# Kernel optimization log

Measured on AMD Instinct MI355X. Metric: run time of the kernel, lower is better.

## Reference

```python
import jax, jax.numpy as jnp
import numpy as np

B, S, H, NH = 2, 2048, 1024, 16
HD = H // NH
ROTARY_DIM = 64
EPS = 1e-5
MINUS_INF = -10000.0


def _apply_rotary(q, k, rotary_dim):
    # q, k: [B, S, NH, HD]; GPT-NeoX style rotate_half on first rotary_dim dims
    pos = jnp.arange(S, dtype=jnp.float32)
    inv_freq = 1.0 / (10000.0 ** (jnp.arange(0, rotary_dim, 2, dtype=jnp.float32) / rotary_dim))
    freqs = pos[:, None] * inv_freq[None, :]                      # [S, rd/2]
    cos = jnp.concatenate([jnp.cos(freqs)] * 2, -1)[None, :, None, :]  # [1,S,1,rd]
    sin = jnp.concatenate([jnp.sin(freqs)] * 2, -1)[None, :, None, :]

    def rot(t):
        t_rot, t_pass = t[..., :rotary_dim], t[..., rotary_dim:]
        t1, t2 = jnp.split(t_rot, 2, axis=-1)
        rotated = jnp.concatenate([-t2, t1], axis=-1)
        return jnp.concatenate([t_rot * cos + rotated * sin, t_pass], axis=-1)

    return rot(q), rot(k)


def setup_inputs() -> dict:
    key = jax.random.key(0)
    ks = jax.random.split(key, 6)
    w_scale = 0.02
    return {
        "x": jax.random.normal(ks[0], (B, S, H), jnp.float32),
        "input_mask": jnp.ones((B, S), jnp.int32),
        "norm_w": jnp.ones((H,), jnp.float32),
        "norm_b": jnp.zeros((H,), jnp.float32),
        "attn_qkvw": jax.random.normal(ks[1], (H, 3 * H), jnp.float32) * w_scale,
        "attn_qkvb": jax.random.normal(ks[2], (3 * H,), jnp.float32) * w_scale,
        "attn_ow": jax.random.normal(ks[3], (H, H), jnp.float32) * w_scale,
        "attn_ob": jax.random.normal(ks[4], (H,), jnp.float32) * w_scale,
    }


def reference(x, input_mask, norm_w, norm_b, attn_qkvw, attn_qkvb, attn_ow, attn_ob):
    # pre-layernorm (qkv_gemm path with config.pre_layer_norm)
    mu = x.mean(-1, keepdims=True)
    var = x.var(-1, keepdims=True)
    xn = (x - mu) * jax.lax.rsqrt(var + EPS) * norm_w + norm_b

    # fused QKV projection
    qkv = xn @ attn_qkvw + attn_qkvb                       # [B,S,3H]
    q, k, v = jnp.split(qkv, 3, axis=-1)
    q = q.reshape(B, S, NH, HD)
    k = k.reshape(B, S, NH, HD)
    v = v.reshape(B, S, NH, HD)

    # rotary embedding on q,k
    q, k = _apply_rotary(q, k, ROTARY_DIM)

    # scaled scores + mask bias (1 - mask) * -10000 + triangular masking
    scale = 1.0 / np.sqrt(HD).astype(np.float32)
    scores = jnp.einsum("bqhd,bkhd->bhqk", q, k) * scale   # [B,NH,S,S]
    mask_bias = (1.0 - input_mask.astype(scores.dtype)) * MINUS_INF
    scores = scores + mask_bias[:, None, None, :]
    causal = jnp.tril(jnp.ones((S, S), bool))
    scores = jnp.where(causal[None, None], scores, MINUS_INF)

    probs = jax.nn.softmax(scores, axis=-1)
    ctx = jnp.einsum("bhqk,bkhd->bqhd", probs, v).reshape(B, S, H)

    # output projection (vector_matmul + bias)
    return ctx @ attn_ow + attn_ob
```

## Files before the change

kernel.cpp:

```cpp
#include <hip/hip_runtime.h>
#include <hip/hip_bf16.h>

#define B_  2
#define S_  2048
#define H_  1024
#define NH_ 16
#define HD_ 64
#define T_  (B_*S_)
#define H3_ (3*H_)

typedef float  floatx4 __attribute__((ext_vector_type(4)));
typedef __bf16 bf16x8  __attribute__((ext_vector_type(8)));

__device__ inline unsigned short f2bf_rn(float f) {
    union { float f; unsigned int u; } v; v.f = f;
    unsigned int u = v.u;
    u += 0x7fffu + ((u >> 16) & 1u);
    return (unsigned short)(u >> 16);
}
__device__ inline floatx4 fzero4() { floatx4 v; v[0]=0.f; v[1]=0.f; v[2]=0.f; v[3]=0.f; return v; }

__device__ inline float bf2f(unsigned short u) {
    union { unsigned int i; float f; } x; x.i = ((unsigned int)u) << 16; return x.f;
}

__device__ inline unsigned int cvtpk_bf16(float lo, float hi) {
    unsigned int r;
    asm("v_cvt_pk_bf16_f32 %0, %1, %2" : "=v"(r) : "v"(lo), "v"(hi));
    return r;
}
__device__ inline float bfsum2(unsigned int u) {
    union { unsigned int i; float f; } a, c;
    a.i = u << 16; c.i = u & 0xffff0000u;
    return a.f + c.f;
}

__device__ inline void gload_lds16(const unsigned short* g, unsigned short* l) {
    __builtin_amdgcn_global_load_lds((const __attribute__((address_space(1))) unsigned int*)g,
                                     (__attribute__((address_space(3))) unsigned int*)l,
                                     16, 0, 0);
}

#define TLD 72
__global__ __launch_bounds__(256) void cvt_both_k(const float* __restrict__ qkvw,
                                                  const float* __restrict__ ow,
                                                  unsigned short* __restrict__ qkvwT,
                                                  unsigned short* __restrict__ owT) {
    __shared__ unsigned short Ts[64 * TLD];
    int id = blockIdx.x;
    const float* W; unsigned short* Wt; int N, nb, kb;
    if (id < 768) { W = qkvw; Wt = qkvwT; N = H3_; nb = (id % 48) * 64; kb = (id / 48) * 64; }
    else { id -= 768; W = ow; Wt = owT; N = H_; nb = (id % 16) * 64; kb = (id / 16) * 64; }
    const int K = H_;
    const int tid = threadIdx.x;
    #pragma unroll
    for (int p = 0; p < 4; p++) {
        const int krow = kb + p * 16 + (tid >> 4);
        const int ncol = (tid & 15) * 4;
        const float4 w = *reinterpret_cast<const float4*>(&W[(size_t)krow * N + nb + ncol]);
        Ts[(ncol + 0) * TLD + p * 16 + (tid >> 4)] = f2bf_rn(w.x);
        Ts[(ncol + 1) * TLD + p * 16 + (tid >> 4)] = f2bf_rn(w.y);
        Ts[(ncol + 2) * TLD + p * 16 + (tid >> 4)] = f2bf_rn(w.z);
        Ts[(ncol + 3) * TLD + p * 16 + (tid >> 4)] = f2bf_rn(w.w);
    }
    __syncthreads();
    #pragma unroll
    for (int p = 0; p < 2; p++) {
        const int n = (tid >> 3) + p * 32;
        const int k8 = (tid & 7) * 8;
        const uint4 v = *reinterpret_cast<const uint4*>(&Ts[n * TLD + k8]);
        *reinterpret_cast<uint4*>(&Wt[(size_t)(nb + n) * K + kb + k8]) = v;
    }
}

__global__ __launch_bounds__(256) void layernorm_k(const float* __restrict__ x,
                                                   const float* __restrict__ w,
                                                   const float* __restrict__ b,
                                                   unsigned short* __restrict__ xn) {
    const int t   = blockIdx.x;
    const int tid = threadIdx.x;
    const float4 v = reinterpret_cast<const float4*>(x + (size_t)t * H_)[tid];
    float s  = v.x + v.y + v.z + v.w;
    float s2 = v.x*v.x + v.y*v.y + v.z*v.z + v.w*v.w;
    for (int off = 32; off > 0; off >>= 1) {
        s  += __shfl_down(s,  off, 64);
        s2 += __shfl_down(s2, off, 64);
    }
    __shared__ float red[8];
    const int wave = tid >> 6, lane = tid & 63;
    if (lane == 0) { red[wave] = s; red[4 + wave] = s2; }
    __syncthreads();
    if (tid == 0) {
        red[0] = red[0] + red[1] + red[2] + red[3];
        red[4] = red[4] + red[5] + red[6] + red[7];
    }
    __syncthreads();
    const float mean = red[0] * (1.f / H_);
    const float var  = red[4] * (1.f / H_) - mean * mean;
    const float rstd = rsqrtf(var + 1e-5f);
    const float4 wv = reinterpret_cast<const float4*>(w)[tid];
    const float4 bv = reinterpret_cast<const float4*>(b)[tid];
    ushort4 o = make_ushort4(f2bf_rn((v.x - mean) * rstd * wv.x + bv.x),
                             f2bf_rn((v.y - mean) * rstd * wv.y + bv.y),
                             f2bf_rn((v.z - mean) * rstd * wv.z + bv.z),
                             f2bf_rn((v.w - mean) * rstd * wv.w + bv.w));
    reinterpret_cast<ushort4*>(xn + (size_t)t * H_)[tid] = o;
}

#define BM 128
#define BN 128

__device__ inline void gemm_core(const unsigned short* __restrict__ A,
                                 const unsigned short* __restrict__ Bt,
                                 int K, int mBase, int nBase,
                                 int tid, floatx4 acc[4][4],
                                 unsigned short* As0, unsigned short* As1,
                                 unsigned short* Bs0, unsigned short* Bs1) {
    const int lane = tid & 63;
    const int wave = tid >> 6;
    const int wr = wave >> 1, wc = wave & 1;
    const int srow = lane >> 2;
    const int scol = (lane & 3) * 8;
    const int mrow = lane & 15;
    const int koff = (lane >> 4) * 8;

    for (int kb = 0; kb < K; kb += 64) {
        __syncthreads();
        #pragma unroll
        for (int p = 0; p < 2; p++) {
            const int r = wave * 16 + p * 64;
            const size_t ga = (size_t)(mBase + r + srow) * K + kb + scol;
            const size_t gb = (size_t)(nBase + r + srow) * K + kb + scol;
            gload_lds16(&A [ga],      &As0[r * 32]);
            gload_lds16(&A [ga + 32], &As1[r * 32]);
            gload_lds16(&Bt[gb],      &Bs0[r * 32]);
            gload_lds16(&Bt[gb + 32], &Bs1[r * 32]);
        }
        __syncthreads();

        #pragma unroll
        for (int half = 0; half < 2; half++) {
            const unsigned short* As = half ? As1 : As0;
            const unsigned short* Bs = half ? Bs1 : Bs0;
            bf16x8 afrag[4], bfrag[4];
            #pragma unroll
            for (int mt = 0; mt < 4; mt++)
                afrag[mt] = *reinterpret_cast<const bf16x8*>(&As[(wr * 64 + mt * 16 + mrow) * 32 + koff]);
            #pragma unroll
            for (int nt = 0; nt < 4; nt++)
                bfrag[nt] = *reinterpret_cast<const bf16x8*>(&Bs[(wc * 64 + nt * 16 + mrow) * 32 + koff]);
            #pragma unroll
            for (int mt = 0; mt < 4; mt++)
                #pragma unroll
                for (int nt = 0; nt < 4; nt++)
                    acc[mt][nt] = __builtin_amdgcn_mfma_f32_16x16x32_bf16(afrag[mt], bfrag[nt], acc[mt][nt], 0, 0, 0);
        }
    }
}

__global__ __launch_bounds__(256) void gemm_qkv_k(const unsigned short* __restrict__ A,
                                                  const unsigned short* __restrict__ Bt,
                                                  const float* __restrict__ bias,
                                                  unsigned short* __restrict__ Qo,
                                                  unsigned short* __restrict__ Ko,
                                                  unsigned short* __restrict__ Vto) {
    __shared__ unsigned short As0[BM * 32], As1[BM * 32];
    __shared__ unsigned short Bs0[BN * 32], Bs1[BN * 32];

    const int tid  = threadIdx.x;
    const int lane = tid & 63;
    const int wave = tid >> 6;
    const int wr = wave >> 1, wc = wave & 1;
    const int mBase = blockIdx.y * BM;
    const int nBase = blockIdx.x * BN;

    floatx4 acc[4][4];
    #pragma unroll
    for (int i = 0; i < 4; i++)
        #pragma unroll
        for (int j = 0; j < 4; j++) acc[i][j] = fzero4();

    gemm_core(A, Bt, H_, mBase, nBase, tid, acc, As0, As1, Bs0, Bs1);

    const int col0 = lane & 15;
    const int r0   = (lane >> 4) * 4;
    const int hg   = (nBase + wc * 64) >> 6;
    const int sec  = hg >> 4;
    const int h    = hg & 15;

    float bs[4];
    #pragma unroll
    for (int nt = 0; nt < 4; nt++) bs[nt] = bias[nBase + wc * 64 + nt * 16 + col0];

    if (sec < 2) {
        unsigned short* dst = (sec == 0) ? Qo : Ko;
        const float if0 = __expf((float)col0        * (-0.2878231366f));
        const float if1 = __expf((float)(16 + col0) * (-0.2878231366f));
        #pragma unroll
        for (int mt = 0; mt < 4; mt++) {
            #pragma unroll
            for (int reg = 0; reg < 4; reg++) {
                const int t  = mBase + wr * 64 + mt * 16 + r0 + reg;
                const int bb = t >> 11;
                const int s  = t & (S_ - 1);
                float sn0, cs0, sn1, cs1;
                __sincosf((float)s * if0, &sn0, &cs0);
                __sincosf((float)s * if1, &sn1, &cs1);
                const float v0 = acc[mt][0][reg] + bs[0];
                const float v1 = acc[mt][1][reg] + bs[1];
                const float v2 = acc[mt][2][reg] + bs[2];
                const float v3 = acc[mt][3][reg] + bs[3];
                const float o0 = v0 * cs0 - v2 * sn0;
                const float o1 = v1 * cs1 - v3 * sn1;
                const float o2 = v2 * cs0 + v0 * sn0;
                const float o3 = v3 * cs1 + v1 * sn1;
                const size_t rb = ((size_t)(bb * NH_ + h) * S_ + s) * HD_;
                dst[rb +      col0] = f2bf_rn(o0);
                dst[rb + 16 + col0] = f2bf_rn(o1);
                dst[rb + 32 + col0] = f2bf_rn(o2);
                dst[rb + 48 + col0] = f2bf_rn(o3);
            }
        }
    } else {
        #pragma unroll
        for (int mt = 0; mt < 4; mt++) {
            const int t0 = mBase + wr * 64 + mt * 16 + r0;
            const int bb = t0 >> 11;
            const int s0 = t0 & (S_ - 1);
            #pragma unroll
            for (int nt = 0; nt < 4; nt++) {
                const int d = nt * 16 + col0;
                ushort4 o;
                o.x = f2bf_rn(acc[mt][nt][0] + bs[nt]);
                o.y = f2bf_rn(acc[mt][nt][1] + bs[nt]);
                o.z = f2bf_rn(acc[mt][nt][2] + bs[nt]);
                o.w = f2bf_rn(acc[mt][nt][3] + bs[nt]);
                *reinterpret_cast<ushort4*>(&Vto[((size_t)(bb * NH_ + h) * HD_ + d) * S_ + s0]) = o;
            }
        }
    }
}

__global__ __launch_bounds__(256) void gemm_proj_k(const unsigned short* __restrict__ A,
                                                   const unsigned short* __restrict__ Bt,
                                                   const float* __restrict__ bias,
                                                   float* __restrict__ Cf,
                                                   int M, int N, int K) {
    __shared__ unsigned short As0[BM * 32], As1[BM * 32];
    __shared__ unsigned short Bs0[BN * 32], Bs1[BN * 32];

    const int tid  = threadIdx.x;
    const int lane = tid & 63;
    const int wave = tid >> 6;
    const int wr = wave >> 1, wc = wave & 1;
    const int mBase = blockIdx.y * BM;
    const int nBase = blockIdx.x * BN;

    floatx4 acc[4][4];
    #pragma unroll
    for (int i = 0; i < 4; i++)
        #pragma unroll
        for (int j = 0; j < 4; j++) acc[i][j] = fzero4();

    gemm_core(A, Bt, K, mBase, nBase, tid, acc, As0, As1, Bs0, Bs1);

    const int col0 = lane & 15;
    const int r0   = (lane >> 4) * 4;
    #pragma unroll
    for (int mt = 0; mt < 4; mt++) {
        #pragma unroll
        for (int nt = 0; nt < 4; nt++) {
            const int gcol = nBase + wc * 64 + nt * 16 + col0;
            const float bsv = bias[gcol];
            #pragma unroll
            for (int reg = 0; reg < 4; reg++) {
                const int grow = mBase + wr * 64 + mt * 16 + r0 + reg;
                Cf[(size_t)grow * N + gcol] = acc[mt][nt][reg] + bsv;
            }
        }
    }
}

#define ALD 72
#define SCL2 0.1803368801f
#define MNEG -14427.0f

__global__ __launch_bounds__(256, 4) void attn_k(const unsigned short* __restrict__ Q,
                                                 const unsigned short* __restrict__ Kg,
                                                 const unsigned short* __restrict__ Vt,
                                                 const int* __restrict__ mask,
                                                 unsigned short* __restrict__ ctx) {
    const int id = blockIdx.x;
    const int bh = id & 31;
    const int v  = 31 - (id >> 5);
    const int b  = bh >> 4;
    const int h  = bh & 15;
    const int tid  = threadIdx.x;
    const int lane = tid & 63;
    const int wave = tid >> 6;

    __shared__ unsigned short Ks [2][64 * ALD];
    __shared__ unsigned short Vts[2][64 * ALD];
    __shared__ unsigned short Mb [S_];

    const size_t base = (size_t)bh * S_ * HD_;
    const int qbase = v * 64 + wave * 16;
    const int r16  = lane & 15;
    const int koff = (lane >> 4) * 8;
    const int g8   = (lane >> 4) * 8;
    const int qcol = qbase + r16;

    {
        const int k0 = tid * 8;
        const int4 ma = *reinterpret_cast<const int4*>(&mask[b * S_ + k0]);
        const int4 mc = *reinterpret_cast<const int4*>(&mask[b * S_ + k0 + 4]);
        union { unsigned short us[8]; uint4 q; } pk;
        pk.us[0] = f2bf_rn((1.f - (float)ma.x) * MNEG);
        pk.us[1] = f2bf_rn((1.f - (float)ma.y) * MNEG);
        pk.us[2] = f2bf_rn((1.f - (float)ma.z) * MNEG);
        pk.us[3] = f2bf_rn((1.f - (float)ma.w) * MNEG);
        pk.us[4] = f2bf_rn((1.f - (float)mc.x) * MNEG);
        pk.us[5] = f2bf_rn((1.f - (float)mc.y) * MNEG);
        pk.us[6] = f2bf_rn((1.f - (float)mc.z) * MNEG);
        pk.us[7] = f2bf_rn((1.f - (float)mc.w) * MNEG);
        *reinterpret_cast<uint4*>(&Mb[k0]) = pk.q;
    }

    const bf16x8 qf0 = *reinterpret_cast<const bf16x8*>(&Q[base + (size_t)(qbase + r16) * HD_ + koff]);
    const bf16x8 qf1 = *reinterpret_cast<const bf16x8*>(&Q[base + (size_t)(qbase + r16) * HD_ + 32 + koff]);

    floatx4 Ot[4];
    #pragma unroll
    for (int db = 0; db < 4; db++) Ot[db] = fzero4();
    float Lp = 0.f;

    const int srow = tid >> 3;
    const int scol = (tid & 7) * 8;
    const int pi = ((srow & 12) << 1) | (srow & 3) | (((srow >> 4) & 1) << 2);

    uint4 k00, k01, k10, k11, v00, v01, v10, v11;
#define PF_TILE(TT, KR0, KR1, VR0, VR1) do {                                                   \
        const int kb_ = (TT) * 64;                                                             \
        KR0 = *reinterpret_cast<const uint4*>(&Kg[base + (size_t)(kb_ + pi)      * HD_ + scol]); \
        KR1 = *reinterpret_cast<const uint4*>(&Kg[base + (size_t)(kb_ + 32 + pi) * HD_ + scol]); \
        VR0 = *reinterpret_cast<const uint4*>(&Vt[base + (size_t)srow        * S_ + kb_ + scol]);  \
        VR1 = *reinterpret_cast<const uint4*>(&Vt[base + (size_t)(srow + 32) * S_ + kb_ + scol]);  \
    } while (0)
#define PREFETCH_MACRO(MI) do {                                                                \
        const int t0_ = min(2 * (MI), v);                                                      \
        const int t1_ = min(2 * (MI) + 1, v);                                                  \
        PF_TILE(t0_, k00, k01, v00, v01);                                                      \
        PF_TILE(t1_, k10, k11, v10, v11);                                                      \
    } while (0)

    const int nmac = (v + 2) >> 1;
    PREFETCH_MACRO(0);

    for (int mi = 0; mi < nmac; mi++) {
        if (mi) __syncthreads();
        *reinterpret_cast<uint4*>(&Ks [0][ srow       * ALD + scol]) = k00;
        *reinterpret_cast<uint4*>(&Ks [0][(srow + 32) * ALD + scol]) = k01;
        *reinterpret_cast<uint4*>(&Ks [1][ srow       * ALD + scol]) = k10;
        *reinterpret_cast<uint4*>(&Ks [1][(srow + 32) * ALD + scol]) = k11;
        *reinterpret_cast<uint4*>(&Vts[0][ srow       * ALD + scol]) = v00;
        *reinterpret_cast<uint4*>(&Vts[0][(srow + 32) * ALD + scol]) = v01;
        *reinterpret_cast<uint4*>(&Vts[1][ srow       * ALD + scol]) = v10;
        *reinterpret_cast<uint4*>(&Vts[1][(srow + 32) * ALD + scol]) = v11;
        __syncthreads();
        if (mi + 1 < nmac) PREFETCH_MACRO(mi + 1);

        #pragma unroll
        for (int half = 0; half < 2; half++) {
            const int kt = 2 * mi + half;
            if (half && kt > v) continue;
            const int kb = kt * 64;
            const unsigned short* ks = Ks [half];
            const unsigned short* vs = Vts[half];

            const unsigned short* mbp = &Mb[kb + g8];
            const ushort4 b00 = *reinterpret_cast<const ushort4*>(mbp);
            const ushort4 b01 = *reinterpret_cast<const ushort4*>(mbp + 4);
            const ushort4 b10 = *reinterpret_cast<const ushort4*>(mbp + 32);
            const ushort4 b11 = *reinterpret_cast<const ushort4*>(mbp + 36);

            #pragma unroll
            for (int w = 0; w < 2; w++) {
                float p[2][4];
                #pragma unroll
                for (int ab = 0; ab < 2; ab++) {
                    const int nt = w * 2 + ab;
                    const bf16x8 kf0 = *reinterpret_cast<const bf16x8*>(&ks[(nt * 16 + r16) * ALD + koff]);
                    const bf16x8 kf1 = *reinterpret_cast<const bf16x8*>(&ks[(nt * 16 + r16) * ALD + 32 + koff]);
                    floatx4 c = fzero4();
                    c = __builtin_amdgcn_mfma_f32_16x16x32_bf16(kf0, qf0, c, 0, 0, 0);
                    c = __builtin_amdgcn_mfma_f32_16x16x32_bf16(kf1, qf1, c, 0, 0, 0);
                    const ushort4 bb = w ? (ab ? b11 : b10) : (ab ? b01 : b00);
                    const int kbase = kb + w * 32 + ab * 4 + g8;
                    float sc0 = c[0] * SCL2 + bf2f(bb.x);
                    float sc1 = c[1] * SCL2 + bf2f(bb.y);
                    float sc2 = c[2] * SCL2 + bf2f(bb.z);
                    float sc3 = c[3] * SCL2 + bf2f(bb.w);
                    if (kt == v) {
                        if (kbase + 0 > qcol) sc0 = MNEG;
                        if (kbase + 1 > qcol) sc1 = MNEG;
                        if (kbase + 2 > qcol) sc2 = MNEG;
                        if (kbase + 3 > qcol) sc3 = MNEG;
                    }
                    p[ab][0] = exp2f(sc0);
                    p[ab][1] = exp2f(sc1);
                    p[ab][2] = exp2f(sc2);
                    p[ab][3] = exp2f(sc3);
                }
                const unsigned int u0 = cvtpk_bf16(p[0][0], p[0][1]);
                const unsigned int u1 = cvtpk_bf16(p[0][2], p[0][3]);
                const unsigned int u2 = cvtpk_bf16(p[1][0], p[1][1]);
                const unsigned int u3 = cvtpk_bf16(p[1][2], p[1][3]);
                Lp += (bfsum2(u0) + bfsum2(u1)) + (bfsum2(u2) + bfsum2(u3));
                union { uint4 u; bf16x8 v; } pf;
                pf.u.x = u0; pf.u.y = u1; pf.u.z = u2; pf.u.w = u3;
                #pragma unroll
                for (int db = 0; db < 4; db++) {
                    const bf16x8 vf = *reinterpret_cast<const bf16x8*>(&vs[(db * 16 + r16) * ALD + w * 32 + koff]);
                    Ot[db] = __builtin_amdgcn_mfma_f32_16x16x32_bf16(vf, pf.v, Ot[db], 0, 0, 0);
                }
            }
        }
    }
#undef PREFETCH_MACRO
#undef PF_TILE

    float lsum = Lp;
    lsum += __shfl_xor(lsum, 16, 64);
    lsum += __shfl_xor(lsum, 32, 64);
    const float rl = 1.f / lsum;
    const int r4 = (lane >> 4) * 4;
    #pragma unroll
    for (int db = 0; db < 4; db++) {
        ushort4 o;
        o.x = f2bf_rn(Ot[db][0] * rl);
        o.y = f2bf_rn(Ot[db][1] * rl);
        o.z = f2bf_rn(Ot[db][2] * rl);
        o.w = f2bf_rn(Ot[db][3] * rl);
        *reinterpret_cast<ushort4*>(&ctx[((size_t)b * S_ + qcol) * H_ + h * HD_ + db * 16 + r4]) = o;
    }
}

extern "C" void kernel_launch(void* const* d_in, const int* in_sizes, int n_in,
                              void* d_out, int out_size, void* d_ws, size_t ws_size,
                              hipStream_t stream) {
    const float* x     = (const float*)d_in[0];
    const int*   mask  = (const int*)d_in[1];
    const float* normw = (const float*)d_in[2];
    const float* normb = (const float*)d_in[3];
    const float* qkvw  = (const float*)d_in[4];
    const float* qkvb  = (const float*)d_in[5];
    const float* ow    = (const float*)d_in[6];
    const float* ob    = (const float*)d_in[7];
    float* out = (float*)d_out;

    char* ws = (char*)d_ws;
    unsigned short* xn_bf   = (unsigned short*)(ws);
    unsigned short* qkvwT   = (unsigned short*)(ws + (8ull  << 20));
    unsigned short* owT     = (unsigned short*)(ws + (14ull << 20));
    unsigned short* Qb      = (unsigned short*)(ws + (16ull << 20));
    unsigned short* Kb      = (unsigned short*)(ws + (24ull << 20));
    unsigned short* Vtb     = (unsigned short*)(ws + (32ull << 20));
    unsigned short* ctx_bf  = (unsigned short*)(ws + (40ull << 20));

    cvt_both_k<<<1024, 256, 0, stream>>>(qkvw, ow, qkvwT, owT);
    layernorm_k<<<T_, 256, 0, stream>>>(x, normw, normb, xn_bf);
    gemm_qkv_k<<<dim3(H3_ / BN, T_ / BM), 256, 0, stream>>>(xn_bf, qkvwT, qkvb, Qb, Kb, Vtb);
    attn_k<<<1024, 256, 0, stream>>>(Qb, Kb, Vtb, mask, ctx_bf);
    gemm_proj_k<<<dim3(H_ / BN, T_ / BM), 256, 0, stream>>>(ctx_bf, owT, ob, out, T_, H_, H_);
}
```

Measured before the change: 197.2 us.

## Shrink projection GEMM tiles and compute softmax row sums via MFMA

```diff
diff --git a/kernel.cpp b/kernel.cpp
--- a/kernel.cpp
+++ b/kernel.cpp
@@ -28,11 +28,6 @@
     unsigned int r;
     asm("v_cvt_pk_bf16_f32 %0, %1, %2" : "=v"(r) : "v"(lo), "v"(hi));
     return r;
-}
-__device__ inline float bfsum2(unsigned int u) {
-    union { unsigned int i; float f; } a, c;
-    a.i = u << 16; c.i = u & 0xffff0000u;
-    return a.f + c.f;
 }
 
 __device__ inline void gload_lds16(const unsigned short* g, unsigned short* l) {
@@ -246,35 +241,73 @@
                                                    const float* __restrict__ bias,
                                                    float* __restrict__ Cf,
                                                    int M, int N, int K) {
-    __shared__ unsigned short As0[BM * 32], As1[BM * 32];
-    __shared__ unsigned short Bs0[BN * 32], Bs1[BN * 32];
+    __shared__ unsigned short As0[128 * 32], As1[128 * 32];
+    __shared__ unsigned short Bs0[ 64 * 32], Bs1[ 64 * 32];
 
     const int tid  = threadIdx.x;
     const int lane = tid & 63;
     const int wave = tid >> 6;
-    const int wr = wave >> 1, wc = wave & 1;
-    const int mBase = blockIdx.y * BM;
-    const int nBase = blockIdx.x * BN;
-
-    floatx4 acc[4][4];
-    #pragma unroll
-    for (int i = 0; i < 4; i++)
+    const int mBase = blockIdx.y * 128;
+    const int nBase = blockIdx.x * 64;
+
+    const int srow = lane >> 2;
+    const int scol = (lane & 3) * 8;
+    const int mrow = lane & 15;
+    const int koff = (lane >> 4) * 8;
+
+    floatx4 acc[2][4];
+    #pragma unroll
+    for (int i = 0; i < 2; i++)
         #pragma unroll
         for (int j = 0; j < 4; j++) acc[i][j] = fzero4();
 
-    gemm_core(A, Bt, K, mBase, nBase, tid, acc, As0, As1, Bs0, Bs1);
+    for (int kb = 0; kb < K; kb += 64) {
+        __syncthreads();
+        #pragma unroll
+        for (int p = 0; p < 2; p++) {
+            const int r = wave * 16 + p * 64;
+            const size_t ga = (size_t)(mBase + r + srow) * K + kb + scol;
+            gload_lds16(&A[ga],      &As0[r * 32]);
+            gload_lds16(&A[ga + 32], &As1[r * 32]);
+        }
+        {
+            const int r = wave * 16;
+            const size_t gb = (size_t)(nBase + r + srow) * K + kb + scol;
+            gload_lds16(&Bt[gb],      &Bs0[r * 32]);
+            gload_lds16(&Bt[gb + 32], &Bs1[r * 32]);
+        }
+        __syncthreads();
+
+        #pragma unroll
+        for (int half = 0; half < 2; half++) {
+            const unsigned short* As = half ? As1 : As0;
+            const unsigned short* Bs = half ? Bs1 : Bs0;
+            bf16x8 afrag[2], bfrag[4];
+            #pragma unroll
+            for (int mt = 0; mt < 2; mt++)
+                afrag[mt] = *reinterpret_cast<const bf16x8*>(&As[(wave * 32 + mt * 16 + mrow) * 32 + koff]);
+            #pragma unroll
+            for (int nt = 0; nt < 4; nt++)
+                bfrag[nt] = *reinterpret_cast<const bf16x8*>(&Bs[(nt * 16 + mrow) * 32 + koff]);
+            #pragma unroll
+            for (int mt = 0; mt < 2; mt++)
+                #pragma unroll
+                for (int nt = 0; nt < 4; nt++)
+                    acc[mt][nt] = __builtin_amdgcn_mfma_f32_16x16x32_bf16(afrag[mt], bfrag[nt], acc[mt][nt], 0, 0, 0);
+        }
+    }
 
     const int col0 = lane & 15;
     const int r0   = (lane >> 4) * 4;
     #pragma unroll
-    for (int mt = 0; mt < 4; mt++) {
+    for (int mt = 0; mt < 2; mt++) {
         #pragma unroll
         for (int nt = 0; nt < 4; nt++) {
-            const int gcol = nBase + wc * 64 + nt * 16 + col0;
+            const int gcol = nBase + nt * 16 + col0;
             const float bsv = bias[gcol];
             #pragma unroll
             for (int reg = 0; reg < 4; reg++) {
-                const int grow = mBase + wr * 64 + mt * 16 + r0 + reg;
+                const int grow = mBase + wave * 32 + mt * 16 + r0 + reg;
                 Cf[(size_t)grow * N + gcol] = acc[mt][nt][reg] + bsv;
             }
         }
@@ -329,10 +362,14 @@
     const bf16x8 qf0 = *reinterpret_cast<const bf16x8*>(&Q[base + (size_t)(qbase + r16) * HD_ + koff]);
     const bf16x8 qf1 = *reinterpret_cast<const bf16x8*>(&Q[base + (size_t)(qbase + r16) * HD_ + 32 + koff]);
 
+    bf16x8 onesA;
+    #pragma unroll
+    for (int q = 0; q < 8; q++) onesA[q] = (__bf16)1.f;
+
     floatx4 Ot[4];
     #pragma unroll
     for (int db = 0; db < 4; db++) Ot[db] = fzero4();
-    float Lp = 0.f;
+    floatx4 Lacc = fzero4();
 
     const int srow = tid >> 3;
     const int scol = (tid & 7) * 8;
@@ -411,28 +448,26 @@
                     p[ab][2] = exp2f(sc2);
                     p[ab][3] = exp2f(sc3);
                 }
-                const unsigned int u0 = cvtpk_bf16(p[0][0], p[0][1]);
-                const unsigned int u1 = cvtpk_bf16(p[0][2], p[0][3]);
-                const unsigned int u2 = cvtpk_bf16(p[1][0], p[1][1]);
-                const unsigned int u3 = cvtpk_bf16(p[1][2], p[1][3]);
-                Lp += (bfsum2(u0) + bfsum2(u1)) + (bfsum2(u2) + bfsum2(u3));
                 union { uint4 u; bf16x8 v; } pf;
-                pf.u.x = u0; pf.u.y = u1; pf.u.z = u2; pf.u.w = u3;
+                pf.u.x = cvtpk_bf16(p[0][0], p[0][1]);
+                pf.u.y = cvtpk_bf16(p[0][2], p[0][3]);
+                pf.u.z = cvtpk_bf16(p[1][0], p[1][1]);
+                pf.u.w = cvtpk_bf16(p[1][2], p[1][3]);
+                __builtin_amdgcn_s_setprio(1);
                 #pragma unroll
                 for (int db = 0; db < 4; db++) {
                     const bf16x8 vf = *reinterpret_cast<const bf16x8*>(&vs[(db * 16 + r16) * ALD + w * 32 + koff]);
                     Ot[db] = __builtin_amdgcn_mfma_f32_16x16x32_bf16(vf, pf.v, Ot[db], 0, 0, 0);
                 }
+                Lacc = __builtin_amdgcn_mfma_f32_16x16x32_bf16(onesA, pf.v, Lacc, 0, 0, 0);
+                __builtin_amdgcn_s_setprio(0);
             }
         }
     }
 #undef PREFETCH_MACRO
 #undef PF_TILE
 
-    float lsum = Lp;
-    lsum += __shfl_xor(lsum, 16, 64);
-    lsum += __shfl_xor(lsum, 32, 64);
-    const float rl = 1.f / lsum;
+    const float rl = 1.f / Lacc[0];
     const int r4 = (lane >> 4) * 4;
     #pragma unroll
     for (int db = 0; db < 4; db++) {
@@ -471,5 +506,5 @@
     layernorm_k<<<T_, 256, 0, stream>>>(x, normw, normb, xn_bf);
     gemm_qkv_k<<<dim3(H3_ / BN, T_ / BM), 256, 0, stream>>>(xn_bf, qkvwT, qkvb, Qb, Kb, Vtb);
     attn_k<<<1024, 256, 0, stream>>>(Qb, Kb, Vtb, mask, ctx_bf);
-    gemm_proj_k<<<dim3(H_ / BN, T_ / BM), 256, 0, stream>>>(ctx_bf, owT, ob, out, T_, H_, H_);
-}
+    gemm_proj_k<<<dim3(H_ / 64, T_ / 128), 256, 0, stream>>>(ctx_bf, owT, ob, out, T_, H_, H_);
+}
```

Result: faster. 191.0 us (-3.2%).
